# Kernel optimization log

Measured on AMD Instinct MI355X. Metric: run time of the kernel, lower is better.

Reference implementation:

```python
import jax, jax.numpy as jnp
import numpy as np

N, D, K = 65536, 512, 5


def setup_inputs() -> dict:
    key = jax.random.key(0)
    k0, k1, k2, k3, k4 = jax.random.split(key, 5)
    x = jax.random.normal(k0, (N, D), dtype=jnp.float32)
    is_protected = jax.random.randint(k1, (N,), 0, 2) > 0  # bool mask
    alpha_p = jax.random.uniform(k2, (D,), dtype=jnp.float32, minval=0.9, maxval=1.1)
    classif_w = jax.random.normal(k3, (K, 1), dtype=jnp.float32)
    centroids = jax.random.normal(k4, (K, D), dtype=jnp.float32)
    return {"x": x, "is_protected": is_protected, "alpha_p": alpha_p,
            "classif_w": classif_w, "centroids": centroids}


def reference(x, is_protected, alpha_p, classif_w, centroids):
    # NOTE: original torch forward applies alpha_p to both the protected and
    # non-protected rows (alpha_np is unused), so the mask split is a no-op
    # and we compute the mapping over all rows at once.
    # distances: sum_d alpha_d * (x_nd - c_kd)^2  -> (n, k)
    diff2 = (x[:, None, :] - centroids[None, :, :]) ** 2  # (n, k, d)
    dist = jnp.einsum("nkd,d->nk", diff2, alpha_p)
    mapping = jax.nn.softmax(dist, axis=-1)              # (n, k)
    reconstructed = mapping @ centroids                  # (n, d)
    pred = (mapping @ jax.nn.sigmoid(classif_w)).ravel() # (n,)
    return mapping, reconstructed, pred
```

## Files before the change

### kernel.cpp

```cpp
#include <hip/hip_runtime.h>
#include <math.h>

#define LFR_N 65536
#define LFR_D 512
#define LFR_K 5
#define RPW   16
#define WPB   4
#define NCH   (LFR_D / 64)
#define BLOCKS (LFR_N / (RPW * WPB))


#define LGKM0() do { asm volatile("s_waitcnt lgkmcnt(0)" ::: "memory"); \
                     __builtin_amdgcn_sched_barrier(0); } while (0)

__global__ __launch_bounds__(256) void lfr_kernel(
    const float* __restrict__ x,
    const float* __restrict__ alpha,
    const float* __restrict__ w,
    const float* __restrict__ cent,
    float* __restrict__ out_map,
    float* __restrict__ out_rec,
    float* __restrict__ out_pred)
{
    __shared__ float  sc[LFR_K][LFR_D];
    __shared__ float  sa[LFR_D];
    __shared__ float4 sx[WPB][16][16];

    const int tid  = threadIdx.x;
    const int lane = tid & 63;
    const int wib  = tid >> 6;
    const int rr   = lane & 15;
    const int qq   = lane >> 4;

    {
        const float4* csrc = (const float4*)cent;
        float4* cdst = (float4*)&sc[0][0];
        #pragma unroll
        for (int i = 0; i < 3; ++i) {
            int idx = tid + i * 256;
            if (idx < (LFR_K * LFR_D) / 4) cdst[idx] = csrc[idx];
        }
        if (tid < LFR_D / 4) ((float4*)sa)[tid] = ((const float4*)alpha)[tid];
    }
    float sigw[LFR_K];
    #pragma unroll
    for (int k = 0; k < LFR_K; ++k) sigw[k] = 1.0f / (1.0f + __expf(-w[k]));
    __syncthreads();

    const int r0 = (blockIdx.x * WPB + wib) * RPW;

    float4 pf[4];
    #pragma unroll
    for (int i = 0; i < 4; ++i)
        pf[i] = *(const float4*)(x + (size_t)(r0 + i*4 + qq) * LFR_D + rr*4);

    float dacc[LFR_K] = {0.f, 0.f, 0.f, 0.f, 0.f};

    #pragma unroll
    for (int ch = 0; ch < NCH; ++ch) {
        if (ch) LGKM0();
        #pragma unroll
        for (int i = 0; i < 4; ++i) {
            const int row = i*4 + qq;
            sx[wib][row][rr ^ row] = pf[i];
        }
        if (ch + 1 < NCH) {
            #pragma unroll
            for (int i = 0; i < 4; ++i)
                pf[i] = *(const float4*)(x + (size_t)(r0 + i*4 + qq) * LFR_D
                                           + (ch + 1) * 64 + rr*4);
        }
        LGKM0();
        #pragma unroll
        for (int j4 = 0; j4 < 4; ++j4) {
            const int col4 = qq*4 + j4;
            float4 xv = sx[wib][rr][col4 ^ rr];
            float4 av = ((const float4*)&sa[ch * 64])[col4];
            #pragma unroll
            for (int k = 0; k < LFR_K; ++k) {
                float4 cv = ((const float4*)&sc[k][ch * 64])[col4];
                float d0 = xv.x - cv.x, d1 = xv.y - cv.y;
                float d2 = xv.z - cv.z, d3 = xv.w - cv.w;
                dacc[k] = fmaf(av.x * d0, d0, dacc[k]);
                dacc[k] = fmaf(av.y * d1, d1, dacc[k]);
                dacc[k] = fmaf(av.z * d2, d2, dacc[k]);
                dacc[k] = fmaf(av.w * d3, d3, dacc[k]);
            }
        }
    }

    #pragma unroll
    for (int k = 0; k < LFR_K; ++k) {
        dacc[k] += __shfl_xor(dacc[k], 16);
        dacc[k] += __shfl_xor(dacc[k], 32);
    }

    float e[LFR_K];
    float mx = dacc[0];
    #pragma unroll
    for (int k = 1; k < LFR_K; ++k) mx = fmaxf(mx, dacc[k]);
    float sum = 0.f;
    #pragma unroll
    for (int k = 0; k < LFR_K; ++k) { e[k] = __expf(dacc[k] - mx); sum += e[k]; }
    float inv = 1.0f / sum;
    #pragma unroll
    for (int k = 0; k < LFR_K; ++k) e[k] *= inv;

    if (qq == 0) {
        float* mp = out_map + (size_t)(r0 + rr) * LFR_K;
        #pragma unroll
        for (int k = 0; k < LFR_K; ++k) mp[k] = e[k];
        float pr = e[0] * sigw[0];
        #pragma unroll
        for (int k = 1; k < LFR_K; ++k) pr = fmaf(e[k], sigw[k], pr);
        out_pred[r0 + rr] = pr;
    }

    #pragma unroll
    for (int ch = 0; ch < NCH; ++ch) {
        LGKM0();
        #pragma unroll
        for (int j4 = 0; j4 < 4; ++j4) {
            const int col4 = qq*4 + j4;
            float4 c0 = ((const float4*)&sc[0][ch * 64])[col4];
            float4 rv;
            rv.x = e[0] * c0.x; rv.y = e[0] * c0.y;
            rv.z = e[0] * c0.z; rv.w = e[0] * c0.w;
            #pragma unroll
            for (int k = 1; k < LFR_K; ++k) {
                float4 cv = ((const float4*)&sc[k][ch * 64])[col4];
                rv.x = fmaf(e[k], cv.x, rv.x);
                rv.y = fmaf(e[k], cv.y, rv.y);
                rv.z = fmaf(e[k], cv.z, rv.z);
                rv.w = fmaf(e[k], cv.w, rv.w);
            }
            sx[wib][rr][col4 ^ rr] = rv;
        }
        LGKM0();
        #pragma unroll
        for (int i = 0; i < 4; ++i) {
            const int row = i*4 + qq;
            float4 v = sx[wib][row][rr ^ row];
            *(float4*)(out_rec + (size_t)(r0 + row) * LFR_D + ch * 64 + rr*4) = v;
        }
    }
}

extern "C" void kernel_launch(void* const* d_in, const int* in_sizes, int n_in,
                              void* d_out, int out_size, void* d_ws, size_t ws_size,
                              hipStream_t stream) {
    const float* x     = (const float*)d_in[0];
    const float* alpha = (const float*)d_in[2];
    const float* w     = (const float*)d_in[3];
    const float* cent  = (const float*)d_in[4];

    float* out   = (float*)d_out;
    float* o_map = out;
    float* o_rec = out + (size_t)LFR_N * LFR_K;
    float* o_prd = out + (size_t)LFR_N * LFR_K + (size_t)LFR_N * LFR_D;

    dim3 grid(BLOCKS), block(256);
    lfr_kernel<<<grid, block, 0, stream>>>(x, alpha, w, cent, o_map, o_rec, o_prd);
}
```

Measured before the change: 248.0 us.

## Stream x tiles directly into LDS with double-buffered global_load_lds

Replaces the register prefetch followed by an LDS store with asynchronous global-to-LDS loads (global_load_lds, 16 bytes per lane). Each lane's source column is pre-swizzled so the existing XOR layout is preserved. Two LDS buffers per wave keep two chunks in flight, synchronised with vmcnt waits instead of lgkmcnt. The goal is to hide global memory latency and cut VGPR and LDS-store traffic. The risk is that the compiler may not order earlier LDS reads of a buffer before the async refill, and the per-wave LDS footprint doubles.

```diff
diff --git a/kernel.cpp b/kernel.cpp
--- a/kernel.cpp
+++ b/kernel.cpp
@@ -12,6 +12,15 @@
 
 #define LGKM0() do { asm volatile("s_waitcnt lgkmcnt(0)" ::: "memory"); \
                      __builtin_amdgcn_sched_barrier(0); } while (0)
+#define WAITVM4() do { asm volatile("s_waitcnt vmcnt(4)" ::: "memory"); \
+                       __builtin_amdgcn_sched_barrier(0); } while (0)
+#define WAITVM0() do { asm volatile("s_waitcnt vmcnt(0)" ::: "memory"); \
+                       __builtin_amdgcn_sched_barrier(0); } while (0)
+
+#define GL2LDS(gaddr, laddr) \
+    __builtin_amdgcn_global_load_lds( \
+        (const __attribute__((address_space(1))) void*)(gaddr), \
+        (__attribute__((address_space(3))) void*)(laddr), 16, 0, 0)
 
 __global__ __launch_bounds__(256) void lfr_kernel(
     const float* __restrict__ x,
@@ -24,13 +33,14 @@
 {
     __shared__ float  sc[LFR_K][LFR_D];
     __shared__ float  sa[LFR_D];
-    __shared__ float4 sx[WPB][16][16];
+    __shared__ float4 sx[WPB][2][16][16];
 
     const int tid  = threadIdx.x;
     const int lane = tid & 63;
     const int wib  = tid >> 6;
     const int rr   = lane & 15;
     const int qq   = lane >> 4;
+    const int ss   = lane & 15;
 
     {
         const float4* csrc = (const float4*)cent;
@@ -49,32 +59,33 @@
 
     const int r0 = (blockIdx.x * WPB + wib) * RPW;
 
-    float4 pf[4];
-    #pragma unroll
-    for (int i = 0; i < 4; ++i)
-        pf[i] = *(const float4*)(x + (size_t)(r0 + i*4 + qq) * LFR_D + rr*4);
+    const float* xw = x + (size_t)r0 * LFR_D;
+
+    #define STAGE(ch, b)                                                        \
+        do {                                                                    \
+            _Pragma("unroll")                                                   \
+            for (int i_ = 0; i_ < 4; ++i_) {                                    \
+                const int row_ = i_ * 4 + qq;                                   \
+                const int cf4_ = ss ^ row_;                                     \
+                GL2LDS(xw + (size_t)row_ * LFR_D + (ch) * 64 + cf4_ * 4,        \
+                       &sx[wib][b][i_ * 4][0]);                                 \
+            }                                                                   \
+        } while (0)
+
+    STAGE(0, 0);
+    STAGE(1, 1);
 
     float dacc[LFR_K] = {0.f, 0.f, 0.f, 0.f, 0.f};
 
     #pragma unroll
     for (int ch = 0; ch < NCH; ++ch) {
-        if (ch) LGKM0();
-        #pragma unroll
-        for (int i = 0; i < 4; ++i) {
-            const int row = i*4 + qq;
-            sx[wib][row][rr ^ row] = pf[i];
-        }
-        if (ch + 1 < NCH) {
-            #pragma unroll
-            for (int i = 0; i < 4; ++i)
-                pf[i] = *(const float4*)(x + (size_t)(r0 + i*4 + qq) * LFR_D
-                                           + (ch + 1) * 64 + rr*4);
-        }
-        LGKM0();
+        if (ch < NCH - 1) WAITVM4();
+        else              WAITVM0();
+        const int b = ch & 1;
         #pragma unroll
         for (int j4 = 0; j4 < 4; ++j4) {
-            const int col4 = qq*4 + j4;
-            float4 xv = sx[wib][rr][col4 ^ rr];
+            const int col4 = qq * 4 + j4;
+            float4 xv = sx[wib][b][rr][col4 ^ rr];
             float4 av = ((const float4*)&sa[ch * 64])[col4];
             #pragma unroll
             for (int k = 0; k < LFR_K; ++k) {
@@ -87,6 +98,7 @@
                 dacc[k] = fmaf(av.w * d3, d3, dacc[k]);
             }
         }
+        if (ch + 2 < NCH) STAGE(ch + 2, b);
     }
 
     #pragma unroll
@@ -121,7 +133,7 @@
         LGKM0();
         #pragma unroll
         for (int j4 = 0; j4 < 4; ++j4) {
-            const int col4 = qq*4 + j4;
+            const int col4 = qq * 4 + j4;
             float4 c0 = ((const float4*)&sc[0][ch * 64])[col4];
             float4 rv;
             rv.x = e[0] * c0.x; rv.y = e[0] * c0.y;
@@ -134,14 +146,14 @@
                 rv.z = fmaf(e[k], cv.z, rv.z);
                 rv.w = fmaf(e[k], cv.w, rv.w);
             }
-            sx[wib][rr][col4 ^ rr] = rv;
+            sx[wib][0][rr][col4 ^ rr] = rv;
         }
         LGKM0();
         #pragma unroll
         for (int i = 0; i < 4; ++i) {
-            const int row = i*4 + qq;
-            float4 v = sx[wib][row][rr ^ row];
-            *(float4*)(out_rec + (size_t)(r0 + row) * LFR_D + ch * 64 + rr*4) = v;
+            const int row = i * 4 + qq;
+            float4 v = sx[wib][0][row][rr ^ row];
+            *(float4*)(out_rec + (size_t)(r0 + row) * LFR_D + ch * 64 + rr * 4) = v;
         }
     }
 }
```

Result: no change. 251.4 us (+1.4%).

## Expand squared distance algebraically and drop shared-memory transpose staging

Applied to the files above, without the earlier changes.

Rewrites the distance as -2·alpha·x·c plus a per-centroid constant computed once per block. The x·alpha term is shared across all centroids, and the x² term is dropped because softmax is shift-invariant per row. Each wave now handles 8 rows, with 8 lanes per row reading float4s straight from global memory. This removes the LDS transpose buffer, the explicit lgkmcnt waits and the software prefetch, and adds launch bounds for occupancy 8. The cost is extra block-setup work with two more syncthreads, less explicit latency hiding, and possible cancellation error from the expanded form.

```diff
diff --git a/kernel.cpp b/kernel.cpp
--- a/kernel.cpp
+++ b/kernel.cpp
@@ -4,16 +4,12 @@
 #define LFR_N 65536
 #define LFR_D 512
 #define LFR_K 5
-#define RPW   16
+#define RPW   8
 #define WPB   4
-#define NCH   (LFR_D / 64)
-#define BLOCKS (LFR_N / (RPW * WPB))
+#define BLOCKS (LFR_N / (RPW * WPB * 8) * 8)
+#define NF4   (LFR_D / 4 / 8)
 
-
-#define LGKM0() do { asm volatile("s_waitcnt lgkmcnt(0)" ::: "memory"); \
-                     __builtin_amdgcn_sched_barrier(0); } while (0)
-
-__global__ __launch_bounds__(256) void lfr_kernel(
+__global__ __launch_bounds__(256, 8) void lfr_kernel(
     const float* __restrict__ x,
     const float* __restrict__ alpha,
     const float* __restrict__ w,
@@ -22,15 +18,18 @@
     float* __restrict__ out_rec,
     float* __restrict__ out_pred)
 {
-    __shared__ float  sc[LFR_K][LFR_D];
-    __shared__ float  sa[LFR_D];
-    __shared__ float4 sx[WPB][16][16];
+    __shared__ float sc[LFR_K][LFR_D];
+    __shared__ float sa2[LFR_D];
+    __shared__ float scp[LFR_K][8];
+    __shared__ float scst[LFR_K];
+    __shared__ float ssig[LFR_K];
 
     const int tid  = threadIdx.x;
     const int lane = tid & 63;
     const int wib  = tid >> 6;
-    const int rr   = lane & 15;
-    const int qq   = lane >> 4;
+    const int wid  = blockIdx.x * WPB + wib;
+    const int rq   = lane >> 3;
+    const int q    = lane & 7;
 
     {
         const float4* csrc = (const float4*)cent;
@@ -40,59 +39,59 @@
             int idx = tid + i * 256;
             if (idx < (LFR_K * LFR_D) / 4) cdst[idx] = csrc[idx];
         }
-        if (tid < LFR_D / 4) ((float4*)sa)[tid] = ((const float4*)alpha)[tid];
+        if (tid < LFR_D / 4) {
+            float4 a = ((const float4*)alpha)[tid];
+            a.x *= -2.0f; a.y *= -2.0f; a.z *= -2.0f; a.w *= -2.0f;
+            ((float4*)sa2)[tid] = a;
+        }
     }
-    float sigw[LFR_K];
-    #pragma unroll
-    for (int k = 0; k < LFR_K; ++k) sigw[k] = 1.0f / (1.0f + __expf(-w[k]));
+    __syncthreads();
+    if (tid < LFR_K * 8) {
+        const int k = tid >> 3, part = tid & 7;
+        float s = 0.0f;
+        for (int j = part * 64; j < part * 64 + 64; ++j) {
+            float cc = sc[k][j];
+            s = fmaf(sa2[j] * cc, cc, s);
+        }
+        scp[k][part] = s;
+    }
+    __syncthreads();
+    if (tid < LFR_K) {
+        float s = 0.0f;
+        #pragma unroll
+        for (int p = 0; p < 8; ++p) s += scp[tid][p];
+        scst[tid] = -0.5f * s;
+        ssig[tid] = 1.0f / (1.0f + __expf(-w[tid]));
+    }
     __syncthreads();
 
-    const int r0 = (blockIdx.x * WPB + wib) * RPW;
-
-    float4 pf[4];
-    #pragma unroll
-    for (int i = 0; i < 4; ++i)
-        pf[i] = *(const float4*)(x + (size_t)(r0 + i*4 + qq) * LFR_D + rr*4);
+    const size_t row = (size_t)wid * RPW + rq;
+    const float* xr = x + row * LFR_D + q * 4;
 
     float dacc[LFR_K] = {0.f, 0.f, 0.f, 0.f, 0.f};
-
-    #pragma unroll
-    for (int ch = 0; ch < NCH; ++ch) {
-        if (ch) LGKM0();
+    #pragma unroll 4
+    for (int j = 0; j < NF4; ++j) {
+        float4 xv = *(const float4*)(xr + j * 32);
+        const int dof = j * 32 + q * 4;
+        float4 av = *(const float4*)&sa2[dof];
+        float v0 = av.x * xv.x, v1 = av.y * xv.y;
+        float v2 = av.z * xv.z, v3 = av.w * xv.w;
         #pragma unroll
-        for (int i = 0; i < 4; ++i) {
-            const int row = i*4 + qq;
-            sx[wib][row][rr ^ row] = pf[i];
-        }
-        if (ch + 1 < NCH) {
-            #pragma unroll
-            for (int i = 0; i < 4; ++i)
-                pf[i] = *(const float4*)(x + (size_t)(r0 + i*4 + qq) * LFR_D
-                                           + (ch + 1) * 64 + rr*4);
-        }
-        LGKM0();
-        #pragma unroll
-        for (int j4 = 0; j4 < 4; ++j4) {
-            const int col4 = qq*4 + j4;
-            float4 xv = sx[wib][rr][col4 ^ rr];
-            float4 av = ((const float4*)&sa[ch * 64])[col4];
-            #pragma unroll
-            for (int k = 0; k < LFR_K; ++k) {
-                float4 cv = ((const float4*)&sc[k][ch * 64])[col4];
-                float d0 = xv.x - cv.x, d1 = xv.y - cv.y;
-                float d2 = xv.z - cv.z, d3 = xv.w - cv.w;
-                dacc[k] = fmaf(av.x * d0, d0, dacc[k]);
-                dacc[k] = fmaf(av.y * d1, d1, dacc[k]);
-                dacc[k] = fmaf(av.z * d2, d2, dacc[k]);
-                dacc[k] = fmaf(av.w * d3, d3, dacc[k]);
-            }
+        for (int k = 0; k < LFR_K; ++k) {
+            float4 cv = *(const float4*)&sc[k][dof];
+            dacc[k] = fmaf(cv.x, v0, dacc[k]);
+            dacc[k] = fmaf(cv.y, v1, dacc[k]);
+            dacc[k] = fmaf(cv.z, v2, dacc[k]);
+            dacc[k] = fmaf(cv.w, v3, dacc[k]);
         }
     }
 
     #pragma unroll
     for (int k = 0; k < LFR_K; ++k) {
-        dacc[k] += __shfl_xor(dacc[k], 16);
-        dacc[k] += __shfl_xor(dacc[k], 32);
+        dacc[k] += __shfl_xor(dacc[k], 1);
+        dacc[k] += __shfl_xor(dacc[k], 2);
+        dacc[k] += __shfl_xor(dacc[k], 4);
+        dacc[k] += scst[k];
     }
 
     float e[LFR_K];
@@ -106,43 +105,33 @@
     #pragma unroll
     for (int k = 0; k < LFR_K; ++k) e[k] *= inv;
 
-    if (qq == 0) {
-        float* mp = out_map + (size_t)(r0 + rr) * LFR_K;
+    if (q == 0) {
+        float* mp = out_map + row * LFR_K;
+        *(float4*)(mp) = make_float4(e[0], e[1], e[2], e[3]);
+        mp[4] = e[4];
+        float pr = e[0] * ssig[0];
         #pragma unroll
-        for (int k = 0; k < LFR_K; ++k) mp[k] = e[k];
-        float pr = e[0] * sigw[0];
-        #pragma unroll
-        for (int k = 1; k < LFR_K; ++k) pr = fmaf(e[k], sigw[k], pr);
-        out_pred[r0 + rr] = pr;
+        for (int k = 1; k < LFR_K; ++k) pr = fmaf(e[k], ssig[k], pr);
+        out_pred[row] = pr;
     }
 
-    #pragma unroll
-    for (int ch = 0; ch < NCH; ++ch) {
-        LGKM0();
+    float* rr = out_rec + row * LFR_D + q * 4;
+    #pragma unroll 4
+    for (int j = 0; j < NF4; ++j) {
+        const int dof = j * 32 + q * 4;
+        float4 c0 = *(const float4*)&sc[0][dof];
+        float4 rv;
+        rv.x = e[0] * c0.x; rv.y = e[0] * c0.y;
+        rv.z = e[0] * c0.z; rv.w = e[0] * c0.w;
         #pragma unroll
-        for (int j4 = 0; j4 < 4; ++j4) {
-            const int col4 = qq*4 + j4;
-            float4 c0 = ((const float4*)&sc[0][ch * 64])[col4];
-            float4 rv;
-            rv.x = e[0] * c0.x; rv.y = e[0] * c0.y;
-            rv.z = e[0] * c0.z; rv.w = e[0] * c0.w;
-            #pragma unroll
-            for (int k = 1; k < LFR_K; ++k) {
-                float4 cv = ((const float4*)&sc[k][ch * 64])[col4];
-                rv.x = fmaf(e[k], cv.x, rv.x);
-                rv.y = fmaf(e[k], cv.y, rv.y);
-                rv.z = fmaf(e[k], cv.z, rv.z);
-                rv.w = fmaf(e[k], cv.w, rv.w);
-            }
-            sx[wib][rr][col4 ^ rr] = rv;
+        for (int k = 1; k < LFR_K; ++k) {
+            float4 cv = *(const float4*)&sc[k][dof];
+            rv.x = fmaf(e[k], cv.x, rv.x);
+            rv.y = fmaf(e[k], cv.y, rv.y);
+            rv.z = fmaf(e[k], cv.z, rv.z);
+            rv.w = fmaf(e[k], cv.w, rv.w);
         }
-        LGKM0();
-        #pragma unroll
-        for (int i = 0; i < 4; ++i) {
-            const int row = i*4 + qq;
-            float4 v = sx[wib][row][rr ^ row];
-            *(float4*)(out_rec + (size_t)(r0 + row) * LFR_D + ch * 64 + rr*4) = v;
-        }
+        *(float4*)(rr + j * 32) = rv;
     }
 }
 
```

New measurement: 281.5 us. +13.5%, slower.
